# Kernel optimization log

Hardware: AMD Instinct MI355X
Metric: run time of the kernel (lower is better)

Reference implementation:

```python
import jax, jax.numpy as jnp
import numpy as np

NUM_EXPERTS = 8
HIDDEN = 2048
INTER = 4096
TOKENS = 8192  # divisible by NUM_EXPERTS


def setup_inputs() -> dict:
    key = jax.random.key(0)
    k1, k2, k3 = jax.random.split(key, 3)
    hidden_states = jax.random.normal(k1, (TOKENS, HIDDEN), dtype=jnp.float32)
    gate_up_proj = jax.random.normal(k2, (NUM_EXPERTS, HIDDEN, 2 * INTER), dtype=jnp.float32) * 0.02
    down_proj = jax.random.normal(k3, (NUM_EXPERTS, INTER, HIDDEN), dtype=jnp.float32) * 0.02
    return {"hidden_states": hidden_states, "gate_up_proj": gate_up_proj, "down_proj": down_proj}


def reference(hidden_states, gate_up_proj, down_proj):
    E, H = gate_up_proj.shape[0], gate_up_proj.shape[1]
    x = hidden_states.reshape(E, -1, H)                      # (E, T/E, H)
    gate_up = jnp.einsum('eth,ehf->etf', x, gate_up_proj)    # (E, T/E, 2I)
    gate, up = jnp.split(gate_up, 2, axis=-1)
    acted = up * jax.nn.silu(gate)                           # (E, T/E, I)
    out = jnp.einsum('eti,eih->eth', acted, down_proj)       # (E, T/E, H)
    return out.reshape(-1, H)
```

## Files before the change

kernel.cpp:

```cpp
#include <hip/hip_runtime.h>


#define E_   8
#define H_   2048
#define I_   4096
#define T_   8192
#define TPE  1024

typedef __bf16 bf16x8 __attribute__((ext_vector_type(8)));
typedef float  f32x4  __attribute__((ext_vector_type(4)));

__device__ __forceinline__ unsigned short f2bf(float f) {
  union { float f; unsigned int u; } v; v.f = f;
  unsigned int u = v.u;
  u += 0x7FFFu + ((u >> 16) & 1u);
  return (unsigned short)(u >> 16);
}

__device__ __forceinline__ void async16(const void* g, void* l) {
  __builtin_amdgcn_global_load_lds(
      (__attribute__((address_space(1))) void*)(g),
      (__attribute__((address_space(3))) void*)(l), 16, 0, 0);
}

#define SB0()      __builtin_amdgcn_sched_barrier(0)
#define BAR()      __builtin_amdgcn_s_barrier()
#define WAITLGKM() asm volatile("s_waitcnt lgkmcnt(0)" ::: "memory")
#define WAITVM(n)  asm volatile("s_waitcnt vmcnt(" #n ")" ::: "memory")

__global__ void convert_bf16(const float* __restrict__ src,
                             unsigned short* __restrict__ dst, long n) {
  long i = ((long)blockIdx.x * blockDim.x + threadIdx.x) * 4;
  const long stride = (long)gridDim.x * blockDim.x * 4;
  for (; i < n; i += stride) {
    const float4 v = *(const float4*)&src[i];
    ushort4 o;
    o.x = f2bf(v.x); o.y = f2bf(v.y); o.z = f2bf(v.z); o.w = f2bf(v.w);
    *(ushort4*)&dst[i] = o;
  }
}

template <int K, int NBN, int LDB, bool SILU>
__global__ __launch_bounds__(512, 2)
void gemm_fused(const unsigned short* __restrict__ Aall,
                const float* __restrict__ Ball,
                void* __restrict__ Cout,
                long sA, long sB, long sC) {
  extern __shared__ char smem[];
  constexpr int NT = K / 64;

  const int tid  = threadIdx.x;
  const int wave = tid >> 6;
  const int lane = tid & 63;
  const int lr   = lane & 15;
  const int lq   = lane >> 4;
  const int wid_m = wave >> 2;
  const int wid_n = wave & 3;

  const int nwg = gridDim.x;
  const int bid = blockIdx.x;
  const int wg  = (bid & 7) * (nwg >> 3) + (bid >> 3);
  const int mb  = wg & 3;
  const int tmp = wg >> 2;
  const int nb  = tmp % NBN;
  const int e   = tmp / NBN;

  const unsigned short* A = Aall + (long)e * sA + (long)(mb * 256) * K;
  const float*          B = Ball + (long)e * sB;

  const int stl  = tid >> 3;
  const int scol = ((tid & 7) ^ (stl & 7)) * 8;

  auto stageA = [&](int bi, int q, int kt) {
    const long col = (long)kt * 64 + scol;
    char* l0 = smem + bi * 32768 + q * 16384 + wave * 1024;
    async16(A + (long)(q * 64 + stl) * K + col,        l0);
    async16(A + (long)(128 + q * 64 + stl) * K + col,  l0 + 8192);
  };

  const int stB = tid & 255;
  int colg;
  {
    const int b  = stB >> 7;
    const int r  = stB & 127;
    const int w  = r >> 5;
    const int nf = (r >> 4) & 1;
    const int l4 = stB & 15;
    if (SILU) {
      const int c = w * 32 + b * 16 + l4;
      colg = nb * 128 + c + (nf ? I_ : 0);
    } else {
      colg = nb * 256 + w * 64 + (b * 2 + nf) * 16 + l4;
    }
  }
  const float* Bp = B + colg;
  const int koB = tid >> 8;

  float bvG1[16], bvG2[16];

#define LOADB(BV, G, KT)                                                    \
  do {                                                                      \
    _Pragma("unroll")                                                       \
    for (int uu = 0; uu < 2; ++uu) {                                        \
      const int ko_ = ((G) * 2 + uu) * 2 + koB;                             \
      const float* p_ = Bp + ((long)(KT) * 64 + ko_ * 8) * (long)LDB;       \
      _Pragma("unroll")                                                     \
      for (int j = 0; j < 8; ++j) BV[uu * 8 + j] = p_[j * (long)LDB];       \
    }                                                                       \
  } while (0)

#define WRITEB(BO, BV, G)                                                   \
  do {                                                                      \
    char* LBw_ = smem + 65536 + (BO) * 32768;                               \
    _Pragma("unroll")                                                       \
    for (int uu = 0; uu < 2; ++uu) {                                        \
      const int ko_ = ((G) * 2 + uu) * 2 + koB;                             \
      bf16x8 pk_;                                                           \
      _Pragma("unroll")                                                     \
      for (int j = 0; j < 8; ++j) pk_[j] = (__bf16)BV[uu * 8 + j];          \
      *(bf16x8*)(LBw_ + stB * 128 + ((ko_ ^ (stB & 7)) * 16)) = pk_;        \
    }                                                                       \
  } while (0)

  const int ax0 = ((0 + lq) ^ (lr & 7)) * 16;
  const int ax1 = ((4 + lq) ^ (lr & 7)) * 16;

  f32x4 acc[8][4];
#pragma unroll
  for (int m = 0; m < 8; ++m)
#pragma unroll
    for (int n = 0; n < 4; ++n) acc[m][n] = (f32x4)0.0f;

  const int t1p = (NT > 1) ? 1 : 0;
  LOADB(bvG1, 0, 0);
  LOADB(bvG2, 1, 0);
  stageA(0, 0, 0);
  stageA(0, 1, 0);
  SB0();
  WAITVM(20); SB0();
  WRITEB(0, bvG1, 0);
  WAITVM(4); SB0();
  WRITEB(0, bvG2, 1);
  WAITLGKM(); SB0();
  stageA(1, 0, t1p); SB0();
  LOADB(bvG1, 0, t1p); SB0();
  stageA(1, 1, t1p); SB0();
  LOADB(bvG2, 1, t1p); SB0();
  WAITVM(36); SB0();
  BAR();

#pragma unroll 1
  for (int t = 0; t < NT; ++t) {
    const int cur = t & 1;
    const int bo  = cur ^ 1;
    const char* LA = smem + cur * 32768;
    const char* LB = smem + 65536 + cur * 32768;
    const int t2v = (t + 2 < NT) ? t + 2 : NT - 1;

    bf16x8 a[4][2], b0[2][2], b1[2][2];

#pragma unroll
    for (int mf = 0; mf < 4; ++mf) {
      const int st = wid_m * 64 + mf * 16 + lr;
      a[mf][0] = *(const bf16x8*)(LA + st * 128 + ax0);
      a[mf][1] = *(const bf16x8*)(LA + st * 128 + ax1);
    }
#pragma unroll
    for (int nf = 0; nf < 2; ++nf) {
      const int st = wid_n * 32 + nf * 16 + lr;
      b0[nf][0] = *(const bf16x8*)(LB + st * 128 + ax0);
      b0[nf][1] = *(const bf16x8*)(LB + st * 128 + ax1);
    }
    SB0();
    BAR();
    WAITLGKM(); SB0();
    __builtin_amdgcn_s_setprio(1);
#pragma unroll
    for (int mf = 0; mf < 4; ++mf)
#pragma unroll
      for (int nf = 0; nf < 2; ++nf) {
        acc[mf][nf] = __builtin_amdgcn_mfma_f32_16x16x32_bf16(a[mf][0], b0[nf][0], acc[mf][nf], 0, 0, 0);
        acc[mf][nf] = __builtin_amdgcn_mfma_f32_16x16x32_bf16(a[mf][1], b0[nf][1], acc[mf][nf], 0, 0, 0);
      }
    __builtin_amdgcn_s_setprio(0);
    BAR();

#pragma unroll
    for (int nf = 0; nf < 2; ++nf) {
      const int st = 128 + wid_n * 32 + nf * 16 + lr;
      b1[nf][0] = *(const bf16x8*)(LB + st * 128 + ax0);
      b1[nf][1] = *(const bf16x8*)(LB + st * 128 + ax1);
    }
    stageA(cur, 0, t2v);
    SB0();
    BAR();
    WAITLGKM(); SB0();
    __builtin_amdgcn_s_setprio(1);
#pragma unroll
    for (int mf = 0; mf < 4; ++mf)
#pragma unroll
      for (int nf = 0; nf < 2; ++nf) {
        acc[mf][2 + nf] = __builtin_amdgcn_mfma_f32_16x16x32_bf16(a[mf][0], b1[nf][0], acc[mf][2 + nf], 0, 0, 0);
        acc[mf][2 + nf] = __builtin_amdgcn_mfma_f32_16x16x32_bf16(a[mf][1], b1[nf][1], acc[mf][2 + nf], 0, 0, 0);
      }
    __builtin_amdgcn_s_setprio(0);
    BAR();

#pragma unroll
    for (int mf = 0; mf < 4; ++mf) {
      const int st = 128 + wid_m * 64 + mf * 16 + lr;
      a[mf][0] = *(const bf16x8*)(LA + st * 128 + ax0);
      a[mf][1] = *(const bf16x8*)(LA + st * 128 + ax1);
    }
    SB0();
    WAITVM(20); SB0();
    WRITEB(bo, bvG1, 0);
    WAITLGKM(); SB0();
    LOADB(bvG1, 0, t2v);
    SB0();
    BAR();
    __builtin_amdgcn_s_setprio(1);
#pragma unroll
    for (int mf = 0; mf < 4; ++mf)
#pragma unroll
      for (int nf = 0; nf < 2; ++nf) {
        acc[4 + mf][2 + nf] = __builtin_amdgcn_mfma_f32_16x16x32_bf16(a[mf][0], b1[nf][0], acc[4 + mf][2 + nf], 0, 0, 0);
        acc[4 + mf][2 + nf] = __builtin_amdgcn_mfma_f32_16x16x32_bf16(a[mf][1], b1[nf][1], acc[4 + mf][2 + nf], 0, 0, 0);
      }
    __builtin_amdgcn_s_setprio(0);
    BAR();

    stageA(cur, 1, t2v);
    SB0();
    WAITVM(20); SB0();
    WRITEB(bo, bvG2, 1);
    WAITLGKM(); SB0();
    LOADB(bvG2, 1, t2v);
    SB0();
    BAR();
    __builtin_amdgcn_s_setprio(1);
#pragma unroll
    for (int mf = 0; mf < 4; ++mf)
#pragma unroll
      for (int nf = 0; nf < 2; ++nf) {
        acc[4 + mf][nf] = __builtin_amdgcn_mfma_f32_16x16x32_bf16(a[mf][0], b0[nf][0], acc[4 + mf][nf], 0, 0, 0);
        acc[4 + mf][nf] = __builtin_amdgcn_mfma_f32_16x16x32_bf16(a[mf][1], b0[nf][1], acc[4 + mf][nf], 0, 0, 0);
      }
    __builtin_amdgcn_s_setprio(0);
    BAR();
  }

  if (SILU) {
    unsigned short* Cc = (unsigned short*)Cout + (long)e * sC;
#pragma unroll
    for (int mf = 0; mf < 8; ++mf)
#pragma unroll
      for (int p = 0; p < 2; ++p)
#pragma unroll
        for (int rr = 0; rr < 4; ++rr) {
          const int row = mb * 256 + wid_m * 128 + mf * 16 + lq * 4 + rr;
          const int col = nb * 128 + wid_n * 32 + p * 16 + lr;
          const float g = acc[mf][p * 2][rr];
          const float u = acc[mf][p * 2 + 1][rr];
          Cc[(long)row * I_ + col] = f2bf(u * (g / (1.0f + __expf(-g))));
        }
  } else {
    float* Cc = (float*)Cout + (long)e * sC;
#pragma unroll
    for (int mf = 0; mf < 8; ++mf)
#pragma unroll
      for (int q = 0; q < 4; ++q)
#pragma unroll
        for (int rr = 0; rr < 4; ++rr) {
          const int row = mb * 256 + wid_m * 128 + mf * 16 + lq * 4 + rr;
          const int col = nb * 256 + wid_n * 64 + q * 16 + lr;
          Cc[(long)row * H_ + col] = acc[mf][q][rr];
        }
  }
#undef LOADB
#undef WRITEB
}

extern "C" void kernel_launch(void* const* d_in, const int* in_sizes, int n_in,
                              void* d_out, int out_size, void* d_ws, size_t ws_size,
                              hipStream_t stream) {
  const float* hs = (const float*)d_in[0];
  const float* w1 = (const float*)d_in[1];
  const float* w2 = (const float*)d_in[2];
  float* out = (float*)d_out;
  char* ws = (char*)d_ws;

  const long HB_B  = (long)T_ * H_ * 2;
  const long ACT_B = (long)T_ * I_ * 2;
  if (ws_size < (size_t)(HB_B + ACT_B)) return;

  unsigned short* hiddenB = (unsigned short*)(ws);
  unsigned short* acted   = (unsigned short*)(ws + HB_B);

  hipLaunchKernelGGL(convert_bf16, dim3(2048), dim3(256), 0, stream,
                     hs, hiddenB, (long)T_ * H_);

  hipLaunchKernelGGL((gemm_fused<H_, 32, 2 * I_, true>),
                     dim3(1024), dim3(512), 131072, stream,
                     hiddenB, w1, acted,
                     (long)TPE * H_, (long)H_ * 2 * I_, (long)TPE * I_);

  hipLaunchKernelGGL((gemm_fused<I_, 8, H_, false>),
                     dim3(256), dim3(512), 131072, stream,
                     acted, w2, out,
                     (long)TPE * I_, (long)I_ * H_, (long)TPE * H_);
}
```

Baseline: 585.3 us.

## Load fp32 B tile with 16-byte vector loads and transpose in registers

Replaces the per-thread scalar fp32 B loads (32 scalar loads into two register groups) with eight f32x4 vector loads per thread covering four adjacent columns. The values are transposed in registers into bf16x8 packs before being written to LDS. The LDS swizzle for B reads and the vmcnt wait counts are changed to match the new layout, and the second B stage in the loop is merged into one. This is meant to cut global load instruction count and register pressure, at the risk of LDS bank conflicts from the new write pattern and a changed overlap schedule.

Measured after the change: 525.2 us. -10.3%, faster.

```diff
diff --git a/kernel.cpp b/kernel.cpp
--- a/kernel.cpp
+++ b/kernel.cpp
@@ -78,52 +78,42 @@
     async16(A + (long)(128 + q * 64 + stl) * K + col,  l0 + 8192);
   };
 
-  const int stB = tid & 255;
-  int colg;
+  int colq;
   {
-    const int b  = stB >> 7;
-    const int r  = stB & 127;
+    const int st = 4 * lane;
+    const int b  = st >> 7;
+    const int r  = st & 127;
     const int w  = r >> 5;
     const int nf = (r >> 4) & 1;
-    const int l4 = stB & 15;
-    if (SILU) {
-      const int c = w * 32 + b * 16 + l4;
-      colg = nb * 128 + c + (nf ? I_ : 0);
-    } else {
-      colg = nb * 256 + w * 64 + (b * 2 + nf) * 16 + l4;
-    }
-  }
-  const float* Bp = B + colg;
-  const int koB = tid >> 8;
-
-  float bvG1[16], bvG2[16];
-
-#define LOADB(BV, G, KT)                                                    \
-  do {                                                                      \
-    _Pragma("unroll")                                                       \
-    for (int uu = 0; uu < 2; ++uu) {                                        \
-      const int ko_ = ((G) * 2 + uu) * 2 + koB;                             \
-      const float* p_ = Bp + ((long)(KT) * 64 + ko_ * 8) * (long)LDB;       \
-      _Pragma("unroll")                                                     \
-      for (int j = 0; j < 8; ++j) BV[uu * 8 + j] = p_[j * (long)LDB];       \
-    }                                                                       \
-  } while (0)
-
-#define WRITEB(BO, BV, G)                                                   \
-  do {                                                                      \
-    char* LBw_ = smem + 65536 + (BO) * 32768;                               \
-    _Pragma("unroll")                                                       \
-    for (int uu = 0; uu < 2; ++uu) {                                        \
-      const int ko_ = ((G) * 2 + uu) * 2 + koB;                             \
-      bf16x8 pk_;                                                           \
-      _Pragma("unroll")                                                     \
-      for (int j = 0; j < 8; ++j) pk_[j] = (__bf16)BV[uu * 8 + j];          \
-      *(bf16x8*)(LBw_ + stB * 128 + ((ko_ ^ (stB & 7)) * 16)) = pk_;        \
-    }                                                                       \
-  } while (0)
-
-  const int ax0 = ((0 + lq) ^ (lr & 7)) * 16;
-  const int ax1 = ((4 + lq) ^ (lr & 7)) * 16;
+    const int l4 = st & 15;
+    if (SILU) colq = nb * 128 + (w * 32 + b * 16 + l4) + (nf ? I_ : 0);
+    else      colq = nb * 256 + w * 64 + (b * 2 + nf) * 16 + l4;
+  }
+  const float* Bq = B + colq;
+
+  f32x4 bv[8];
+  auto LOADB = [&](int kt) {
+    const long kbase = (long)kt * 64 + wave * 8;
+#pragma unroll
+    for (int i = 0; i < 8; ++i)
+      bv[i] = *(const f32x4*)&Bq[(kbase + i) * (long)LDB];
+  };
+  auto WRITEB = [&](int bo) {
+    char* LBw = smem + 65536 + bo * 32768;
+    const int slot = wave ^ (lane & 7);
+#pragma unroll
+    for (int j = 0; j < 4; ++j) {
+      bf16x8 pk;
+#pragma unroll
+      for (int i = 0; i < 8; ++i) pk[i] = (__bf16)bv[i][j];
+      const int st = 4 * lane + j;
+      *(bf16x8*)(LBw + st * 128 + slot * 16) = pk;
+    }
+  };
+
+  const int axA0 = ((0 + lq) ^ (lr & 7)) * 16;
+  const int axA1 = ((4 + lq) ^ (lr & 7)) * 16;
+  const int bxn[2] = { (lr >> 2), 4 + (lr >> 2) };
 
   f32x4 acc[8][4];
 #pragma unroll
@@ -132,21 +122,17 @@
     for (int n = 0; n < 4; ++n) acc[m][n] = (f32x4)0.0f;
 
   const int t1p = (NT > 1) ? 1 : 0;
-  LOADB(bvG1, 0, 0);
-  LOADB(bvG2, 1, 0);
+  LOADB(0);
   stageA(0, 0, 0);
   stageA(0, 1, 0);
   SB0();
-  WAITVM(20); SB0();
-  WRITEB(0, bvG1, 0);
   WAITVM(4); SB0();
-  WRITEB(0, bvG2, 1);
+  WRITEB(0);
   WAITLGKM(); SB0();
   stageA(1, 0, t1p); SB0();
-  LOADB(bvG1, 0, t1p); SB0();
+  LOADB(t1p); SB0();
   stageA(1, 1, t1p); SB0();
-  LOADB(bvG2, 1, t1p); SB0();
-  WAITVM(36); SB0();
+  WAITVM(12); SB0();
   BAR();
 
 #pragma unroll 1
@@ -162,14 +148,14 @@
 #pragma unroll
     for (int mf = 0; mf < 4; ++mf) {
       const int st = wid_m * 64 + mf * 16 + lr;
-      a[mf][0] = *(const bf16x8*)(LA + st * 128 + ax0);
-      a[mf][1] = *(const bf16x8*)(LA + st * 128 + ax1);
+      a[mf][0] = *(const bf16x8*)(LA + st * 128 + axA0);
+      a[mf][1] = *(const bf16x8*)(LA + st * 128 + axA1);
     }
 #pragma unroll
     for (int nf = 0; nf < 2; ++nf) {
       const int st = wid_n * 32 + nf * 16 + lr;
-      b0[nf][0] = *(const bf16x8*)(LB + st * 128 + ax0);
-      b0[nf][1] = *(const bf16x8*)(LB + st * 128 + ax1);
+      b0[nf][0] = *(const bf16x8*)(LB + st * 128 + ((0 + lq) ^ bxn[nf]) * 16);
+      b0[nf][1] = *(const bf16x8*)(LB + st * 128 + ((4 + lq) ^ bxn[nf]) * 16);
     }
     SB0();
     BAR();
@@ -188,8 +174,8 @@
 #pragma unroll
     for (int nf = 0; nf < 2; ++nf) {
       const int st = 128 + wid_n * 32 + nf * 16 + lr;
-      b1[nf][0] = *(const bf16x8*)(LB + st * 128 + ax0);
-      b1[nf][1] = *(const bf16x8*)(LB + st * 128 + ax1);
+      b1[nf][0] = *(const bf16x8*)(LB + st * 128 + ((0 + lq) ^ bxn[nf]) * 16);
+      b1[nf][1] = *(const bf16x8*)(LB + st * 128 + ((4 + lq) ^ bxn[nf]) * 16);
     }
     stageA(cur, 0, t2v);
     SB0();
@@ -209,14 +195,14 @@
 #pragma unroll
     for (int mf = 0; mf < 4; ++mf) {
       const int st = 128 + wid_m * 64 + mf * 16 + lr;
-      a[mf][0] = *(const bf16x8*)(LA + st * 128 + ax0);
-      a[mf][1] = *(const bf16x8*)(LA + st * 128 + ax1);
-    }
-    SB0();
-    WAITVM(20); SB0();
-    WRITEB(bo, bvG1, 0);
+      a[mf][0] = *(const bf16x8*)(LA + st * 128 + axA0);
+      a[mf][1] = *(const bf16x8*)(LA + st * 128 + axA1);
+    }
+    SB0();
+    WAITVM(4); SB0();
+    WRITEB(bo);
     WAITLGKM(); SB0();
-    LOADB(bvG1, 0, t2v);
+    LOADB(t2v);
     SB0();
     BAR();
     __builtin_amdgcn_s_setprio(1);
@@ -232,11 +218,7 @@
 
     stageA(cur, 1, t2v);
     SB0();
-    WAITVM(20); SB0();
-    WRITEB(bo, bvG2, 1);
-    WAITLGKM(); SB0();
-    LOADB(bvG2, 1, t2v);
-    SB0();
+    WAITVM(12); SB0();
     BAR();
     __builtin_amdgcn_s_setprio(1);
 #pragma unroll
@@ -249,6 +231,8 @@
     __builtin_amdgcn_s_setprio(0);
     BAR();
   }
+
+  WAITVM(0);
 
   if (SILU) {
     unsigned short* Cc = (unsigned short*)Cout + (long)e * sC;
@@ -277,8 +261,6 @@
           Cc[(long)row * H_ + col] = acc[mf][q][rr];
         }
   }
-#undef LOADB
-#undef WRITEB
 }
 
 extern "C" void kernel_launch(void* const* d_in, const int* in_sizes, int n_in,
```
